# Kernel tuning notes

Measured on AMD Instinct MI355X. Metric: run time of the kernel, lower is better.

The kernel has to match this reference:

```python
import jax, jax.numpy as jnp
import numpy as np

B, C_IN, C_OUT, E, K = 4, 32, 64, 200000, 5


def setup_inputs() -> dict:
    key = jax.random.key(0)
    k1, k2, k3, k4 = jax.random.split(key, 4)
    x = jax.random.normal(k1, (B, C_IN, E), dtype=jnp.float32)
    # Gi: per-edge [self_id, n1, n2, n3, n4] one-ring indices into the edge axis
    Gi = jax.random.randint(k2, (B, E, K), 0, E, dtype=jnp.int32)
    # Conv2d(C_IN, C_OUT, kernel_size=(1, K)) weights, PyTorch layout (O, I, 1, K)
    fan_in = C_IN * K
    bound = 1.0 / np.sqrt(fan_in)
    W = jax.random.uniform(k3, (C_OUT, C_IN, 1, K), jnp.float32, -bound, bound)
    b = jax.random.uniform(k4, (C_OUT,), jnp.float32, -bound, bound)
    return {"x": x, "Gi": Gi, "W": W, "b": b}


def _mesh_conv(x, Gi, W, b):
    Bn, C, En = x.shape
    # prepend zero-padding column (index 0 after Gi+1 maps to zeros)
    xp = jnp.concatenate([jnp.zeros((Bn, C, 1), x.dtype), x], axis=2)  # (B, C, E+1)
    idx = Gi.astype(jnp.int32) + 1  # (B, E, 5)
    # gather 1-ring neighbor features: f[b, c, e, j] = xp[b, c, idx[b, e, j]]
    f = jax.vmap(lambda xb, ib: xb[:, ib])(xp, idx)  # (B, C, E, 5)
    f0, f1, f2, f3, f4 = (f[..., j] for j in range(5))
    # symmetric, order-invariant combine
    G = jnp.stack([f0, f1 + f3, f2 + f4, jnp.abs(f1 - f3), jnp.abs(f2 - f4)], axis=3)
    # Conv2d with kernel (1, K), no padding -> contraction over (C_in, K)
    out = jnp.einsum('bcek,ock->boe', G, W[:, :, 0, :]) + b[None, :, None]
    return out[..., None]  # (B, C_out, E, 1)


def reference(x, Gi, W, b):
    return _mesh_conv(x, Gi, W, b)
```

## Files before the change

### kernel.cpp

```cpp
#include <hip/hip_runtime.h>

typedef unsigned int u32;
typedef __bf16 bf16x8 __attribute__((ext_vector_type(8)));
typedef float f32x4 __attribute__((ext_vector_type(4)));

#define B_DIM 4
#define E_DIM 200000
#define C_OUT 64
#define TPB   12500
#define NT    (B_DIM * TPB)
#define NBLK  1024
#define NW    (NBLK * 4)
#define WLDS_U4 1792

__device__ __forceinline__ u32 pack_bf2(float lo, float hi) {
  u32 a = __float_as_uint(lo) + 0x8000u;
  u32 b = __float_as_uint(hi) + 0x8000u;
  return __builtin_amdgcn_perm(b, a, 0x07060302u);
}

__device__ __forceinline__ u32 absdiff_pack(u32 a, u32 b) {
  float alo = __uint_as_float(a << 16), ahi = __uint_as_float(a & 0xffff0000u);
  float blo = __uint_as_float(b << 16), bhi = __uint_as_float(b & 0xffff0000u);
  u32 dlo = __float_as_uint(alo - blo) + 0x8000u;
  u32 dhi = __float_as_uint(ahi - bhi) + 0x8000u;
  return __builtin_amdgcn_perm(dhi, dlo, 0x07060302u) & 0x7fff7fffu;
}

__device__ __forceinline__ uint4 absdiff_vec(uint4 a, uint4 b) {
  return make_uint4(absdiff_pack(a.x, b.x), absdiff_pack(a.y, b.y),
                    absdiff_pack(a.z, b.z), absdiff_pack(a.w, b.w));
}

__global__ __launch_bounds__(256) void xpose_kernel(const float* __restrict__ x,
                                                    u32* __restrict__ xT) {
  __shared__ u32 T[256 * 17];
  const int b = blockIdx.y;
  const int e0 = blockIdx.x * 256;
  const int t = threadIdx.x;
  const int nrows = min(256, E_DIM - e0);
  const float* xb = x + (size_t)b * 32 * E_DIM + e0;
  if (t < nrows) {
#pragma unroll
    for (int u = 0; u < 16; ++u) {
      const float lo = xb[(size_t)(2 * u) * E_DIM + t];
      const float hi = xb[(size_t)(2 * u + 1) * E_DIM + t];
      T[t * 17 + u] = pack_bf2(lo, hi);
    }
  }
  __syncthreads();
  const int total = nrows * 16;
  u32* dst = xT + ((size_t)b * E_DIM + e0) * 16;
#pragma unroll
  for (int k = 0; k < 16; ++k) {
    const int g = t + k * 256;
    if (g < total) dst[g] = T[(g >> 4) * 17 + (g & 15)];
  }
}

__global__ __launch_bounds__(256) void mesh_main(const u32* __restrict__ xT,
                                                 const int* __restrict__ Gi,
                                                 const float* __restrict__ W,
                                                 const float* __restrict__ bias,
                                                 float* __restrict__ out) {
  __shared__ uint4 Wl[WLDS_U4];
  __shared__ float Bl[64];

  {
    u32* wl = (u32*)&Wl[0];
#pragma unroll
    for (int k = 0; k < 28; ++k) {
      const int p = (int)threadIdx.x + k * 256;
      const int r = p & 3;
      const int o = (p >> 2) & 63;
      const int qq = (p >> 8) & 3;
      const int s = p >> 10;
      const int kk = s < 3 ? s : s - 2;
      const int c0 = qq * 8 + 2 * r;
      const float w0 = W[(o * 32 + c0) * 5 + kk];
      const float w1 = W[(o * 32 + c0 + 1) * 5 + kk];
      wl[p] = pack_bf2(w0, w1);
    }
    if (threadIdx.x < 64) Bl[threadIdx.x] = bias[threadIdx.x];
  }
  __syncthreads();

  const int l = (int)threadIdx.x & 63;
  const int wv = (int)threadIdx.x >> 6;
  const int n = l & 15;
  const int q = l >> 4;

  const uint4* xb4 = (const uint4*)xT;

  int t = blockIdx.x * 4 + wv;

  int gcur[5], gnext[5];
  {
    const int b = t / TPB;
    const int e = (t - b * TPB) * 16 + n;
    const int* gp = Gi + (b * E_DIM + e) * 5;
#pragma unroll
    for (int s = 0; s < 5; ++s) gcur[s] = b * E_DIM + gp[s];
  }
  uint4 cur[5];
#pragma unroll
  for (int s = 0; s < 5; ++s) cur[s] = xb4[(size_t)gcur[s] * 4 + q];

  int t1 = t + NW;
  if (t1 < NT) {
    const int b = t1 / TPB;
    const int e = (t1 - b * TPB) * 16 + n;
    const int* gp = Gi + (b * E_DIM + e) * 5;
#pragma unroll
    for (int s = 0; s < 5; ++s) gnext[s] = b * E_DIM + gp[s];
  }

  for (;;) {
    const bool has = t1 < NT;
    uint4 nxt[5];
    if (has) {
#pragma unroll
      for (int s = 0; s < 5; ++s) nxt[s] = xb4[(size_t)gnext[s] * 4 + q];
    }
    const int t2 = t1 + NW;
    if (t2 < NT) {
      const int b = t2 / TPB;
      const int e = (t2 - b * TPB) * 16 + n;
      const int* gp = Gi + (b * E_DIM + e) * 5;
#pragma unroll
      for (int s = 0; s < 5; ++s) gnext[s] = b * E_DIM + gp[s];
    }

    union U { uint4 u; bf16x8 v; };
    U frag[7];
#pragma unroll
    for (int s = 0; s < 5; ++s) frag[s].u = cur[s];
    frag[5].u = absdiff_vec(cur[1], cur[3]);
    frag[6].u = absdiff_vec(cur[2], cur[4]);

    f32x4 acc0 = *(const f32x4*)&Bl[0 * 16 + q * 4];
    f32x4 acc1 = *(const f32x4*)&Bl[1 * 16 + q * 4];
    f32x4 acc2 = *(const f32x4*)&Bl[2 * 16 + q * 4];
    f32x4 acc3 = *(const f32x4*)&Bl[3 * 16 + q * 4];
#pragma unroll
    for (int c = 0; c < 7; ++c) {
      const uint4* wp = Wl + (c * 4 + q) * 64 + n;
      U a0, a1;
      a0.u = wp[0];
      a1.u = wp[16];
      acc0 = __builtin_amdgcn_mfma_f32_16x16x32_bf16(a0.v, frag[c].v, acc0, 0, 0, 0);
      acc1 = __builtin_amdgcn_mfma_f32_16x16x32_bf16(a1.v, frag[c].v, acc1, 0, 0, 0);
      a0.u = wp[32];
      a1.u = wp[48];
      acc2 = __builtin_amdgcn_mfma_f32_16x16x32_bf16(a0.v, frag[c].v, acc2, 0, 0, 0);
      acc3 = __builtin_amdgcn_mfma_f32_16x16x32_bf16(a1.v, frag[c].v, acc3, 0, 0, 0);
    }

    {
      const int b = t / TPB;
      const int e0 = (t - b * TPB) * 16;
      float* ob = out + ((size_t)(b * C_OUT + q * 4) * E_DIM + e0 + n);
#pragma unroll
      for (int r = 0; r < 4; ++r) {
        ob[(size_t)(0 * 16 + r) * E_DIM] = acc0[r];
        ob[(size_t)(1 * 16 + r) * E_DIM] = acc1[r];
        ob[(size_t)(2 * 16 + r) * E_DIM] = acc2[r];
        ob[(size_t)(3 * 16 + r) * E_DIM] = acc3[r];
      }
    }

    if (!has) break;
    t = t1;
    t1 = t2;
#pragma unroll
    for (int s = 0; s < 5; ++s) cur[s] = nxt[s];
  }
}

extern "C" void kernel_launch(void* const* d_in, const int* in_sizes, int n_in,
                              void* d_out, int out_size, void* d_ws, size_t ws_size,
                              hipStream_t stream) {
  const float* x    = (const float*)d_in[0];
  const int*   Gi   = (const int*)d_in[1];
  const float* W    = (const float*)d_in[2];
  const float* bias = (const float*)d_in[3];
  float* out = (float*)d_out;

  u32* xT = (u32*)d_ws;

  dim3 gx((E_DIM + 255) / 256, B_DIM);
  xpose_kernel<<<gx, 256, 0, stream>>>(x, xT);

  mesh_main<<<NBLK, 256, 0, stream>>>(xT, Gi, W, bias, out);
}
```

Measured before the change: 404.4 us.

## Map each batch to a pair of XCDs for gather cache locality

Reassigns blocks so that, assuming round-robin block dispatch across the 8 XCDs, each batch's tiles are processed only by two XCDs. The random neighbor gathers then hit a per-batch 12.8 MB working set instead of the full multi-batch set in each XCD's L2. It also raises the block count to 1280, removes the per-tile batch division, and partially unrolls the weight staging loop. The locality gain relies on the hardware dispatch order matching the blockIdx&7 assumption.

New measurement: 411.7 us. No clear change (+1.8%).

```diff
diff --git a/kernel.cpp b/kernel.cpp
--- a/kernel.cpp
+++ b/kernel.cpp
@@ -8,9 +8,9 @@
 #define E_DIM 200000
 #define C_OUT 64
 #define TPB   12500
-#define NT    (B_DIM * TPB)
-#define NBLK  1024
-#define NW    (NBLK * 4)
+#define NBLK  1280
+#define BPB   (NBLK / B_DIM)
+#define TSTRIDE (BPB * 4)
 #define WLDS_U4 1792
 
 __device__ __forceinline__ u32 pack_bf2(float lo, float hi) {
@@ -68,7 +68,7 @@
 
   {
     u32* wl = (u32*)&Wl[0];
-#pragma unroll
+#pragma unroll 4
     for (int k = 0; k < 28; ++k) {
       const int p = (int)threadIdx.x + k * 256;
       const int r = p & 3;
@@ -90,45 +90,46 @@
   const int n = l & 15;
   const int q = l >> 4;
 
-  const uint4* xb4 = (const uint4*)xT;
+  const int xcd = (int)blockIdx.x & 7;
+  const int blk = (int)blockIdx.x >> 3;
+  const int batch = xcd >> 1;
+  const int idx = (xcd & 1) * (BPB / 2) + blk;
 
-  int t = blockIdx.x * 4 + wv;
+  const uint4* xb4 = (const uint4*)(xT + (size_t)batch * E_DIM * 16);
+  const int* Gib = Gi + (size_t)batch * E_DIM * 5;
+  float* outb = out + (size_t)batch * C_OUT * E_DIM;
+
+  int lt = idx * 4 + wv;
 
   int gcur[5], gnext[5];
   {
-    const int b = t / TPB;
-    const int e = (t - b * TPB) * 16 + n;
-    const int* gp = Gi + (b * E_DIM + e) * 5;
+    const int* gp = Gib + (lt * 16 + n) * 5;
 #pragma unroll
-    for (int s = 0; s < 5; ++s) gcur[s] = b * E_DIM + gp[s];
+    for (int s = 0; s < 5; ++s) gcur[s] = gp[s];
   }
   uint4 cur[5];
 #pragma unroll
   for (int s = 0; s < 5; ++s) cur[s] = xb4[(size_t)gcur[s] * 4 + q];
 
-  int t1 = t + NW;
-  if (t1 < NT) {
-    const int b = t1 / TPB;
-    const int e = (t1 - b * TPB) * 16 + n;
-    const int* gp = Gi + (b * E_DIM + e) * 5;
+  int lt1 = lt + TSTRIDE;
+  if (lt1 < TPB) {
+    const int* gp = Gib + (lt1 * 16 + n) * 5;
 #pragma unroll
-    for (int s = 0; s < 5; ++s) gnext[s] = b * E_DIM + gp[s];
+    for (int s = 0; s < 5; ++s) gnext[s] = gp[s];
   }
 
   for (;;) {
-    const bool has = t1 < NT;
+    const bool has = lt1 < TPB;
     uint4 nxt[5];
     if (has) {
 #pragma unroll
       for (int s = 0; s < 5; ++s) nxt[s] = xb4[(size_t)gnext[s] * 4 + q];
     }
-    const int t2 = t1 + NW;
-    if (t2 < NT) {
-      const int b = t2 / TPB;
-      const int e = (t2 - b * TPB) * 16 + n;
-      const int* gp = Gi + (b * E_DIM + e) * 5;
+    const int lt2 = lt1 + TSTRIDE;
+    if (lt2 < TPB) {
+      const int* gp = Gib + (lt2 * 16 + n) * 5;
 #pragma unroll
-      for (int s = 0; s < 5; ++s) gnext[s] = b * E_DIM + gp[s];
+      for (int s = 0; s < 5; ++s) gnext[s] = gp[s];
     }
 
     union U { uint4 u; bf16x8 v; };
@@ -157,9 +158,7 @@
     }
 
     {
-      const int b = t / TPB;
-      const int e0 = (t - b * TPB) * 16;
-      float* ob = out + ((size_t)(b * C_OUT + q * 4) * E_DIM + e0 + n);
+      float* ob = outb + ((size_t)(q * 4) * E_DIM + lt * 16 + n);
 #pragma unroll
       for (int r = 0; r < 4; ++r) {
         ob[(size_t)(0 * 16 + r) * E_DIM] = acc0[r];
@@ -170,8 +169,8 @@
     }
 
     if (!has) break;
-    t = t1;
-    t1 = t2;
+    lt = lt1;
+    lt1 = lt2;
 #pragma unroll
     for (int s = 0; s < 5; ++s) cur[s] = nxt[s];
   }
```
